# Performance work log

Hardware: AMD Instinct MI355X
Metric: run time of the kernel (lower is better)

## Reference

```python
import jax, jax.numpy as jnp
import numpy as np

D_INP=36; D_MODEL=144; NHEAD=4; NHID=128; NLAYERS=2
MAX_LEN=215; D_STATIC=9; D_PE=16; N_CLASSES=2; B=128
D_OB=D_MODEL//D_INP; GCH=MAX_LEN*D_OB; D_TR=D_MODEL+D_PE; D_FINAL=D_TR+D_INP
_EI=np.stack(np.nonzero(np.ones((D_INP,D_INP),dtype=np.int64)))  # torch.nonzero(ones).T -> all pairs
SRC_N=jnp.asarray(_EI[0]); TGT_N=jnp.asarray(_EI[1]); N_EDGE=_EI.shape[1]


def setup_inputs():
    ks=jax.random.split(jax.random.key(0),40)
    def w(i,shape,s=0.05): return jax.random.normal(ks[i],shape,jnp.float32)*s
    return {
      'src': jax.random.normal(ks[0],(MAX_LEN,B,2*D_INP),jnp.float32),
      'static': jax.random.normal(ks[1],(B,D_STATIC),jnp.float32),
      'times': jax.random.uniform(ks[2],(MAX_LEN,B),jnp.float32)*MAX_LEN,
      'lengths': jax.random.randint(ks[3],(B,),32,MAX_LEN+1),
      'R_u': w(4,(1,D_INP*D_OB)),
      'emb_w': w(5,(D_INP,D_STATIC)), 'emb_b': jnp.zeros(D_INP,jnp.float32),
      'Wv1': w(6,(GCH,GCH),1.0/np.sqrt(GCH)), 'bv1': jnp.zeros(GCH,jnp.float32),
      'Wv2': w(7,(GCH,GCH),1.0/np.sqrt(GCH)), 'bv2': jnp.zeros(GCH,jnp.float32),
      'in_proj_w': w(8,(NLAYERS,3*D_TR,D_TR)), 'in_proj_b': jnp.zeros((NLAYERS,3*D_TR),jnp.float32),
      'out_w': w(9,(NLAYERS,D_TR,D_TR)), 'out_b': jnp.zeros((NLAYERS,D_TR),jnp.float32),
      'lin1_w': w(10,(NLAYERS,NHID,D_TR)), 'lin1_b': jnp.zeros((NLAYERS,NHID),jnp.float32),
      'lin2_w': w(11,(NLAYERS,D_TR,NHID)), 'lin2_b': jnp.zeros((NLAYERS,D_TR),jnp.float32),
      'ln1_s': jnp.ones((NLAYERS,D_TR),jnp.float32), 'ln1_b': jnp.zeros((NLAYERS,D_TR),jnp.float32),
      'ln2_s': jnp.ones((NLAYERS,D_TR),jnp.float32), 'ln2_b': jnp.zeros((NLAYERS,D_TR),jnp.float32),
      'mlp1_w': w(12,(D_FINAL,D_FINAL)), 'mlp1_b': jnp.zeros(D_FINAL,jnp.float32),
      'mlp2_w': w(13,(N_CLASSES,D_FINAL)), 'mlp2_b': jnp.zeros(N_CLASSES,jnp.float32),
    }


def _seg_softmax(wgt, seg, n):
    m=jnp.full((n,),-jnp.inf,wgt.dtype).at[seg].max(wgt)
    e=jnp.exp(wgt-m[seg])
    s=jnp.zeros((n,),wgt.dtype).at[seg].add(e)
    return e/s[seg]


def _ln(x,s,b):
    mu=jnp.mean(x,-1,keepdims=True); v=jnp.var(x,-1,keepdims=True)
    return (x-mu)/jnp.sqrt(v+1e-5)*s+b


def _forward(src, static, times, R_u, emb_w, emb_b, Wv1, bv1, Wv2, bv2, in_proj_w, in_proj_b, out_w, out_b, lin1_w, lin1_b, lin2_w, lin2_b, ln1_s, ln1_b, ln2_s, ln2_b, mlp1_w, mlp1_b, mlp2_w, mlp2_b, lengths):
    T,Bb=src.shape[0],src.shape[1]
    obs=src[:,:,:D_INP]                                  # drop mask half
    h=jax.nn.relu(jnp.repeat(obs,D_OB,axis=-1)*R_u)      # h_u = relu(x_u*R_u), [T,B,144]
    ts=jnp.asarray(MAX_LEN**np.linspace(0,1,D_PE//2),jnp.float32)
    scaled=times[:,:,None]/ts
    pe=jnp.concatenate([jnp.sin(scaled),jnp.cos(scaled)],-1)  # [T,B,16]
    emb=static@emb_w.T+emb_b                             # [B,36]
    # --- Observation_progation x2 (use_beta=False): gather-softmax-scatter per sensor graph ---
    xb=h.transpose(1,0,2).reshape(Bb,T,D_INP,D_OB).transpose(0,2,1,3).reshape(Bb,D_INP,GCH)
    ew=jnp.ones((N_EDGE,),jnp.float32)                   # adj=ones -> edge_weights=1
    gamma=_seg_softmax(ew,TGT_N,D_INP)                   # softmax over edges per target node
    def prop(x_,Wv,bv):
        V=jax.nn.relu(x_@Wv.T+bv)                        # relu(lin_value(x_j))
        msgs=V[:,SRC_N,:]*gamma[None,:,None]             # gather source features per edge
        return jnp.zeros_like(x_).at[:,TGT_N,:].add(msgs)  # scatter-add to targets
    x1=prop(xb,Wv1,bv1)
    x2=prop(x1,Wv2,bv2)                                  # layer2 uses alpha1 = raw edge_weights
    alpha=jnp.broadcast_to(ew[None,:],(Bb,N_EDGE))       # alpha_all.T
    sq=jnp.sum(alpha*alpha,1)
    d2=jnp.maximum(sq[:,None]+sq[None,:]-2.0*(alpha@alpha.T),0.0)
    distance=jnp.mean(jnp.sqrt(d2))
    out=x2.reshape(Bb,D_INP,T,D_OB).transpose(2,0,1,3).reshape(T,Bb,D_INP*D_OB)
    x=jnp.concatenate([out,pe],-1)                       # [T,B,160]
    mask=jnp.arange(T)[None,:]>=lengths[:,None]          # [B,T] True = padded
    hd=D_TR//NHEAD
    for l in range(NLAYERS):                             # torch post-norm TransformerEncoderLayer
        qkv=x@in_proj_w[l].T+in_proj_b[l]
        q,k,v=jnp.split(qkv,3,-1)
        def heads(t): return t.reshape(T,Bb,NHEAD,hd).transpose(1,2,0,3)  # [B,H,T,hd]
        sc=jnp.einsum('bhqd,bhkd->bhqk',heads(q),heads(k))/np.sqrt(hd)
        sc=jnp.where(mask[:,None,None,:],jnp.float32(-1e30),sc)
        o=jnp.einsum('bhqk,bhkd->bhqd',jax.nn.softmax(sc,-1),heads(v))
        o=o.transpose(2,0,1,3).reshape(T,Bb,D_TR)@out_w[l].T+out_b[l]
        x=_ln(x+o,ln1_s[l],ln1_b[l])
        ff=jax.nn.relu(x@lin1_w[l].T+lin1_b[l])@lin2_w[l].T+lin2_b[l]
        x=_ln(x+ff,ln2_s[l],ln2_b[l])
    valid=1.0-mask.T[:,:,None].astype(x.dtype)           # [T,B,1]
    agg=jnp.sum(x*valid,0)/(lengths[:,None].astype(x.dtype)+1.0)
    feat=jnp.concatenate([agg,emb],1)                    # [B,196]
    logits=jax.nn.relu(feat@mlp1_w.T+mlp1_b)@mlp2_w.T+mlp2_b
    return logits,distance


def reference(src, static, times, lengths, R_u, emb_w, emb_b, Wv1, bv1, Wv2, bv2, in_proj_w, in_proj_b, out_w, out_b, lin1_w, lin1_b, lin2_w, lin2_b, ln1_s, ln1_b, ln2_s, ln2_b, mlp1_w, mlp1_b, mlp2_w, mlp2_b):
    return _forward(src, static, times, R_u, emb_w, emb_b, Wv1, bv1, Wv2, bv2, in_proj_w, in_proj_b, out_w, out_b, lin1_w, lin1_b, lin2_w, lin2_b, ln1_s, ln1_b, ln2_s, ln2_b, mlp1_w, mlp1_b, mlp2_w, mlp2_b, lengths)
```

## Files before the change

kernel.cpp:

```cpp
#include <hip/hip_runtime.h>
#include <math.h>

#define T_LEN 215
#define TP    224
#define B_N   128
#define DINP  36
#define D_TR  160
#define HD    40
#define D_FIN 196
#define KPG   864

typedef __attribute__((ext_vector_type(8))) short short8v;
typedef __attribute__((ext_vector_type(4))) float f32x4;

__device__ __forceinline__ ushort f2bf(float x) {
  union { float f; unsigned u; } c; c.f = x;
  unsigned r = c.u + 0x7fffu + ((c.u >> 16) & 1u);
  return (ushort)(r >> 16);
}
__device__ __forceinline__ float bf2f(ushort h) {
  union { unsigned u; float f; } c; c.u = ((unsigned)h) << 16;
  return c.f;
}

__global__ __launch_bounds__(256) void k_prep(const float* __restrict__ Wv1,
    const float* __restrict__ Wv2, const float* __restrict__ ipw, const float* __restrict__ ow,
    const float* __restrict__ l1w, const float* __restrict__ l2w,
    const float* __restrict__ src, const float* __restrict__ R_u,
    const float* __restrict__ stat, const float* __restrict__ emb_w, const float* __restrict__ emb_b,
    ushort* __restrict__ wv1b, ushort* __restrict__ wv2b, ushort* __restrict__ ipwb,
    ushort* __restrict__ owb, ushort* __restrict__ l1wb, ushort* __restrict__ l2wb,
    float* __restrict__ v2acc, float* __restrict__ featacc,
    ushort* __restrict__ obuf16, ushort* __restrict__ xb16) {
  __shared__ float Ss[T_LEN * DINP];
  if (blockIdx.x >= 8202) {
    const int b = blockIdx.x - 8202, tid = threadIdx.x;
    for (int i = tid; i < T_LEN * DINP; i += 256) {
      int t = i / DINP, j = i - t * DINP;
      Ss[i] = src[((size_t)t * B_N + b) * 72 + j];
    }
    __syncthreads();
    for (int i = tid; i < DINP * T_LEN; i += 256) {
      int ii = i / T_LEN, t = i - ii * T_LEN;
      float v = Ss[t * DINP + ii];
      float4 r = ((const float4*)R_u)[ii];
      ushort4 o;
      o.x = f2bf(fmaxf(v * r.x, 0.f)); o.y = f2bf(fmaxf(v * r.y, 0.f));
      o.z = f2bf(fmaxf(v * r.z, 0.f)); o.w = f2bf(fmaxf(v * r.w, 0.f));
      ushort* row = xb16 + (size_t)(b * DINP + ii) * KPG;
      *(ushort4*)(row + 4 * t) = o;
      if (t == 0) { ushort4 z = {0, 0, 0, 0}; *(ushort4*)(row + 860) = z; }
    }
    return;
  }
  int i = blockIdx.x * 256 + threadIdx.x;
  if (i < 746496) { int n = i / KPG, k = i % KPG;
    wv1b[i] = (n < 860 && k < 860) ? f2bf(Wv1[n * 860 + k]) : (ushort)0; return; }
  i -= 746496;
  if (i < 746496) { int n = i / KPG, k = i % KPG;
    wv2b[i] = (n < 860 && k < 860) ? f2bf(Wv2[n * 860 + k]) : (ushort)0; return; }
  i -= 746496;
  if (i < 153600) { ipwb[i] = f2bf(ipw[i]); return; }
  i -= 153600;
  if (i < 51200)  { owb[i] = f2bf(ow[i]); return; }
  i -= 51200;
  if (i < 40960)  { l1wb[i] = f2bf(l1w[i]); return; }
  i -= 40960;
  if (i < 40960)  { l2wb[i] = f2bf(l2w[i]); return; }
  i -= 40960;
  if (i < 110592) { v2acc[i] = 0.f; return; }
  i -= 110592;
  if (i < 20480)  { int b = i / D_TR, d = i - b * D_TR;
    featacc[b * D_FIN + d] = 0.f; return; }
  i -= 20480;
  if (i < 4608)   { int b = i / DINP, ii = i - b * DINP;
    float s = emb_b[ii];
    #pragma unroll
    for (int k = 0; k < 9; k++) s = fmaf(stat[b * 9 + k], emb_w[ii * 9 + k], s);
    featacc[b * D_FIN + D_TR + ii] = s; return; }
  i -= 4608;
  if (i < 184320) {
    int b = i / 1440, rem = i % 1440;
    int t = 215 + rem / 160, cc = rem % 160;
    obuf16[((size_t)b * TP + t) * D_TR + cc] = 0; return;
  }
}

__global__ __launch_bounds__(256) void k_red_s1(const ushort* __restrict__ V1b, ushort* __restrict__ s1) {
  int idx = blockIdx.x * 256 + threadIdx.x;
  if (idx >= B_N * KPG) return;
  int b = idx / KPG, n = idx % KPG;
  float s = 0.f;
  if (n < 860) {
    #pragma unroll 4
    for (int i = 0; i < DINP; i++) s += bf2f(V1b[((size_t)b * DINP + i) * 860 + n]);
    s *= (1.0f / 36.0f);
  }
  s1[idx] = (n < 860) ? f2bf(s) : (ushort)0;
}

__global__ __launch_bounds__(256) void k_buildx(const float* __restrict__ v2acc,
    const float* __restrict__ bv2, const float* __restrict__ times,
    ushort* __restrict__ x16) {
  int idx = blockIdx.x * 256 + threadIdx.x;
  if (idx >= B_N * TP * 40) return;
  int c = idx % 40;
  int r = idx / 40;
  int t = r % TP, b = r / TP;
  float4 f = {0.f, 0.f, 0.f, 0.f};
  if (t < T_LEN) {
    if (c < 36) {
      float4 a = *(const float4*)&v2acc[(size_t)b * KPG + 4 * t];
      float4 bb = *(const float4*)&bv2[4 * t];
      f.x = fmaxf(a.x + bb.x, 0.f); f.y = fmaxf(a.y + bb.y, 0.f);
      f.z = fmaxf(a.z + bb.z, 0.f); f.w = fmaxf(a.w + bb.w, 0.f);
    } else {
      float tm = times[t * B_N + b];
      int j0 = (c - 36) * 4;
      bool is_sin = j0 < 8;
      int kb = j0 & 7;
      float o[4];
      #pragma unroll
      for (int qq = 0; qq < 4; qq++) {
        float ts = expf((float)(kb + qq) * 0.76723400f);
        float sc = tm / ts;
        o[qq] = is_sin ? sinf(sc) : cosf(sc);
      }
      f.x = o[0]; f.y = o[1]; f.z = o[2]; f.w = o[3];
    }
  }
  ushort4 h = {f2bf(f.x), f2bf(f.y), f2bf(f.z), f2bf(f.w)};
  *(ushort4*)(x16 + (size_t)r * D_TR + 4 * c) = h;
}

template <int RELU, int SPLIT, int WMODE, int BNT>
__global__ __launch_bounds__(256) void gemm_bf16(const ushort* __restrict__ A,
    const ushort* __restrict__ W, const float* __restrict__ bias, void* __restrict__ Cv,
    int KP, int ldc, int ncols, int kts) {
  __shared__ ushort As[128 * 32];
  __shared__ ushort Ws[BNT * 32];
  constexpr int NJ = BNT / 16;
  const int tid = threadIdx.x;
  const int wave = tid >> 6, lane = tid & 63;
  const int lr = lane & 15, hi = lane >> 4;
  const int m0 = blockIdx.y * 128, n0 = blockIdx.x * BNT;
  const int kt0 = blockIdx.z * kts;

  f32x4 acc[2][NJ];
  #pragma unroll
  for (int i = 0; i < 2; i++)
    #pragma unroll
    for (int j = 0; j < NJ; j++) acc[i][j] = (f32x4){0.f, 0.f, 0.f, 0.f};

  const int ar = tid >> 2, g = tid & 3;
  const size_t abase0 = (size_t)(m0 + ar) * KP;
  const size_t abase1 = (size_t)(m0 + ar + 64) * KP;
  const size_t bbase0 = (size_t)(n0 + ar) * KP;
  const size_t bbase1 = (size_t)(n0 + ar + 64) * KP;
  const int awb0 = ar * 64 + ((g * 16) ^ ((ar & 3) << 4));
  const int awb1 = awb0 + 64 * 64;

  const int arow0 = wave * 32 + lr;
  const int arb0 = arow0 * 64 + ((hi * 16) ^ ((arow0 & 3) << 4));
  const int arb1 = (arow0 + 16) * 64 + ((hi * 16) ^ (((arow0 + 16) & 3) << 4));
  int brb[NJ];
  #pragma unroll
  for (int j = 0; j < NJ; j++)
    brb[j] = (j * 16 + lr) * 64 + ((hi * 16) ^ ((lr & 3) << 4));

  for (int kt = 0; kt < kts; ++kt) {
    const int k0 = (kt0 + kt) * 32;
    uint4 va0 = *(const uint4*)(A + abase0 + k0 + g * 8);
    uint4 va1 = *(const uint4*)(A + abase1 + k0 + g * 8);
    uint4 vb0 = *(const uint4*)(W + bbase0 + k0 + g * 8);
    uint4 vb1;
    if constexpr (BNT == 128) vb1 = *(const uint4*)(W + bbase1 + k0 + g * 8);
    if (kt) __syncthreads();
    *(uint4*)((char*)As + awb0) = va0;
    *(uint4*)((char*)As + awb1) = va1;
    *(uint4*)((char*)Ws + awb0) = vb0;
    if constexpr (BNT == 128) *(uint4*)((char*)Ws + awb1) = vb1;
    __syncthreads();
    short8v a0 = *(const short8v*)((const char*)As + arb0);
    short8v a1 = *(const short8v*)((const char*)As + arb1);
    #pragma unroll
    for (int j = 0; j < NJ; j++) {
      short8v bf = *(const short8v*)((const char*)Ws + brb[j]);
      acc[0][j] = __builtin_amdgcn_mfma_f32_16x16x32_bf16(a0, bf, acc[0][j], 0, 0, 0);
      acc[1][j] = __builtin_amdgcn_mfma_f32_16x16x32_bf16(a1, bf, acc[1][j], 0, 0, 0);
    }
  }

  #pragma unroll
  for (int i = 0; i < 2; i++) {
    #pragma unroll
    for (int j = 0; j < NJ; j++) {
      int col = n0 + j * 16 + lr;
      int row = m0 + wave * 32 + i * 16 + hi * 4;
      if (col < ncols) {
        if constexpr (SPLIT) {
          #pragma unroll
          for (int r = 0; r < 4; r++)
            atomicAdd((float*)Cv + (size_t)(row + r) * ldc + col, acc[i][j][r]);
        } else {
          float bb = bias ? bias[col] : 0.f;
          #pragma unroll
          for (int r = 0; r < 4; r++) {
            float xv = acc[i][j][r] + bb;
            if (RELU) xv = fmaxf(xv, 0.f);
            if (WMODE == 0) ((float*)Cv)[(size_t)(row + r) * ldc + col] = xv;
            else            ((ushort*)Cv)[(size_t)(row + r) * ldc + col] = f2bf(xv);
          }
        }
      }
    }
  }
}

__global__ __launch_bounds__(256) void gemm_qkv(const ushort* __restrict__ A,
    const ushort* __restrict__ W, const float* __restrict__ bias,
    ushort* __restrict__ qkvB, ushort* __restrict__ Vt, int kts) {
  __shared__ ushort As[128 * 32];
  __shared__ ushort Ws[128 * 32];
  const int KP = 160;
  const int tid = threadIdx.x;
  const int wave = tid >> 6, lane = tid & 63;
  const int lr = lane & 15, hi = lane >> 4;
  const int m0 = blockIdx.y * 128, n0 = blockIdx.x * 128;

  f32x4 acc[2][8];
  #pragma unroll
  for (int i = 0; i < 2; i++)
    #pragma unroll
    for (int j = 0; j < 8; j++) acc[i][j] = (f32x4){0.f, 0.f, 0.f, 0.f};

  const int ar = tid >> 2, g = tid & 3;
  const size_t abase0 = (size_t)(m0 + ar) * KP;
  const size_t abase1 = (size_t)(m0 + ar + 64) * KP;
  const size_t bbase0 = (size_t)(n0 + ar) * KP;
  const size_t bbase1 = (size_t)(n0 + ar + 64) * KP;
  const int awb0 = ar * 64 + ((g * 16) ^ ((ar & 3) << 4));
  const int awb1 = awb0 + 64 * 64;

  const int arow0 = wave * 32 + lr;
  const int arb0 = arow0 * 64 + ((hi * 16) ^ ((arow0 & 3) << 4));
  const int arb1 = (arow0 + 16) * 64 + ((hi * 16) ^ (((arow0 + 16) & 3) << 4));
  int brb[8];
  #pragma unroll
  for (int j = 0; j < 8; j++)
    brb[j] = (j * 16 + lr) * 64 + ((hi * 16) ^ ((lr & 3) << 4));

  for (int kt = 0; kt < kts; ++kt) {
    const int k0 = kt * 32;
    uint4 va0 = *(const uint4*)(A + abase0 + k0 + g * 8);
    uint4 va1 = *(const uint4*)(A + abase1 + k0 + g * 8);
    uint4 vb0 = *(const uint4*)(W + bbase0 + k0 + g * 8);
    uint4 vb1 = *(const uint4*)(W + bbase1 + k0 + g * 8);
    if (kt) __syncthreads();
    *(uint4*)((char*)As + awb0) = va0;
    *(uint4*)((char*)As + awb1) = va1;
    *(uint4*)((char*)Ws + awb0) = vb0;
    *(uint4*)((char*)Ws + awb1) = vb1;
    __syncthreads();
    short8v a0 = *(const short8v*)((const char*)As + arb0);
    short8v a1 = *(const short8v*)((const char*)As + arb1);
    #pragma unroll
    for (int j = 0; j < 8; j++) {
      short8v bf = *(const short8v*)((const char*)Ws + brb[j]);
      acc[0][j] = __builtin_amdgcn_mfma_f32_16x16x32_bf16(a0, bf, acc[0][j], 0, 0, 0);
      acc[1][j] = __builtin_amdgcn_mfma_f32_16x16x32_bf16(a1, bf, acc[1][j], 0, 0, 0);
    }
  }

  #pragma unroll
  for (int i = 0; i < 2; i++) {
    const int row = m0 + wave * 32 + i * 16 + hi * 4;
    const int b = row / TP, t0 = row - b * TP;
    #pragma unroll
    for (int j = 0; j < 8; j++) {
      int col = n0 + j * 16 + lr;
      if (col < 320) {
        float bb = bias[col];
        #pragma unroll
        for (int r = 0; r < 4; r++)
          qkvB[(size_t)(row + r) * 480 + col] = f2bf(acc[i][j][r] + bb);
      } else if (col < 480) {
        float bb = bias[col];
        int dg = col - 320;
        int hh = dg / 40, dd = dg - hh * 40;
        ushort4 pv;
        pv.x = f2bf(acc[i][j][0] + bb); pv.y = f2bf(acc[i][j][1] + bb);
        pv.z = f2bf(acc[i][j][2] + bb); pv.w = f2bf(acc[i][j][3] + bb);
        *(ushort4*)(Vt + (((size_t)(b * 4 + hh) * 48 + dd) * TP + t0)) = pv;
      }
    }
  }
}

__global__ __launch_bounds__(256) void gemm_lnff(const ushort* __restrict__ Ao,
    const ushort* __restrict__ Wo, const float* __restrict__ bo,
    const float* __restrict__ g1, const float* __restrict__ be1,
    const ushort* __restrict__ W1, const float* __restrict__ b1,
    const ushort* __restrict__ W2, const float* __restrict__ b2,
    const float* __restrict__ g2, const float* __restrict__ be2,
    ushort* __restrict__ x16, const int* __restrict__ lengths,
    float* __restrict__ featacc) {
  __shared__ ushort As[64 * 32];
  __shared__ ushort Ws[160 * 32];
  __shared__ ushort W1s[128 * 32];
  __shared__ ushort W2s[160 * 32];
  __shared__ ushort Xln[64 * 168];
  __shared__ ushort Hs[64 * 136];
  const int tid = threadIdx.x;
  const int wave = tid >> 6, lane = tid & 63;
  const int lr = lane & 15, hi = lane >> 4;
  const int m0 = blockIdx.x * 64;

  const int ar = tid >> 2, g = tid & 3;
  const int awb = ar * 64 + ((g * 16) ^ ((ar & 3) << 4));
  const int awb1 = awb + 64 * 64;
  const int wr0 = tid >> 2,         ws0 = tid & 3;
  const int wr1 = (tid + 256) >> 2, ws1 = (tid + 256) & 3;
  const int wr2 = (tid + 512) >> 2, ws2 = (tid + 512) & 3;
  const int wwb0 = wr0 * 64 + ((ws0 * 16) ^ ((wr0 & 3) << 4));
  const int wwb1 = wr1 * 64 + ((ws1 * 16) ^ ((wr1 & 3) << 4));
  const int wwb2 = wr2 * 64 + ((ws2 * 16) ^ ((wr2 & 3) << 4));
  const int arow = wave * 16 + lr;
  const int arb = arow * 64 + ((hi * 16) ^ ((arow & 3) << 4));
  int brb[10];
  #pragma unroll
  for (int j = 0; j < 10; j++)
    brb[j] = (j * 16 + lr) * 64 + ((hi * 16) ^ ((lr & 3) << 4));

  const int lrow0 = wave * 16 + hi * 4;
  const int rb = m0 + lrow0;

  {
    f32x4 acc[10];
    #pragma unroll
    for (int j = 0; j < 10; j++) acc[j] = (f32x4){0.f, 0.f, 0.f, 0.f};
    const size_t abase = (size_t)(m0 + ar) * 160;
    for (int kt = 0; kt < 5; ++kt) {
      const int k0 = kt * 32;
      uint4 va = *(const uint4*)(Ao + abase + k0 + g * 8);
      uint4 w0 = *(const uint4*)(Wo + (size_t)wr0 * 160 + k0 + ws0 * 8);
      uint4 w1 = *(const uint4*)(Wo + (size_t)wr1 * 160 + k0 + ws1 * 8);
      uint4 w2;
      if (tid < 128) w2 = *(const uint4*)(Wo + (size_t)wr2 * 160 + k0 + ws2 * 8);
      if (kt) __syncthreads();
      *(uint4*)((char*)As + awb) = va;
      *(uint4*)((char*)Ws + wwb0) = w0;
      *(uint4*)((char*)Ws + wwb1) = w1;
      if (tid < 128) *(uint4*)((char*)Ws + wwb2) = w2;
      __syncthreads();
      short8v a0 = *(const short8v*)((const char*)As + arb);
      #pragma unroll
      for (int j = 0; j < 10; j++) {
        short8v bf = *(const short8v*)((const char*)Ws + brb[j]);
        acc[j] = __builtin_amdgcn_mfma_f32_16x16x32_bf16(a0, bf, acc[j], 0, 0, 0);
      }
    }
    float s[4] = {0.f, 0.f, 0.f, 0.f};
    #pragma unroll
    for (int j = 0; j < 10; j++) {
      const int col = j * 16 + lr;
      const float bb = bo[col];
      #pragma unroll
      for (int r = 0; r < 4; r++) {
        float v = acc[j][r] + bb + bf2f(x16[(size_t)(rb + r) * D_TR + col]);
        acc[j][r] = v;
        s[r] += v;
      }
    }
    #pragma unroll
    for (int r = 0; r < 4; r++) {
      s[r] += __shfl_xor(s[r], 1, 64);
      s[r] += __shfl_xor(s[r], 2, 64);
      s[r] += __shfl_xor(s[r], 4, 64);
      s[r] += __shfl_xor(s[r], 8, 64);
    }
    float mu[4], q2[4] = {0.f, 0.f, 0.f, 0.f};
    #pragma unroll
    for (int r = 0; r < 4; r++) mu[r] = s[r] * (1.0f / 160.0f);
    #pragma unroll
    for (int j = 0; j < 10; j++)
      #pragma unroll
      for (int r = 0; r < 4; r++) {
        float d = acc[j][r] - mu[r];
        q2[r] += d * d;
      }
    #pragma unroll
    for (int r = 0; r < 4; r++) {
      q2[r] += __shfl_xor(q2[r], 1, 64);
      q2[r] += __shfl_xor(q2[r], 2, 64);
      q2[r] += __shfl_xor(q2[r], 4, 64);
      q2[r] += __shfl_xor(q2[r], 8, 64);
    }
    float rstd[4];
    #pragma unroll
    for (int r = 0; r < 4; r++) rstd[r] = rsqrtf(q2[r] * (1.0f / 160.0f) + 1e-5f);
    #pragma unroll
    for (int j = 0; j < 10; j++) {
      const int col = j * 16 + lr;
      const float gc = g1[col], bc = be1[col];
      #pragma unroll
      for (int r = 0; r < 4; r++) {
        float o = (acc[j][r] - mu[r]) * rstd[r] * gc + bc;
        Xln[(lrow0 + r) * 168 + col] = f2bf(o);
      }
    }
  }
  __syncthreads();

  {
    f32x4 acc1[8];
    #pragma unroll
    for (int j = 0; j < 8; j++) acc1[j] = (f32x4){0.f, 0.f, 0.f, 0.f};
    int brb8[8];
    #pragma unroll
    for (int j = 0; j < 8; j++)
      brb8[j] = (j * 16 + lr) * 64 + ((hi * 16) ^ ((lr & 3) << 4));
    for (int kt = 0; kt < 5; ++kt) {
      const int k0 = kt * 32;
      uint4 w10 = *(const uint4*)(W1 + (size_t)ar * 160 + k0 + g * 8);
      uint4 w11 = *(const uint4*)(W1 + (size_t)(ar + 64) * 160 + k0 + g * 8);
      if (kt) __syncthreads();
      *(uint4*)((char*)W1s + awb) = w10;
      *(uint4*)((char*)W1s + awb1) = w11;
      __syncthreads();
      short8v a0 = *(const short8v*)(&Xln[(wave * 16 + lr) * 168 + k0 + hi * 8]);
      #pragma unroll
      for (int j = 0; j < 8; j++) {
        short8v bf = *(const short8v*)((const char*)W1s + brb8[j]);
        acc1[j] = __builtin_amdgcn_mfma_f32_16x16x32_bf16(a0, bf, acc1[j], 0, 0, 0);
      }
    }
    #pragma unroll
    for (int j = 0; j < 8; j++) {
      const int col = j * 16 + lr;
      const float bb = b1[col];
      #pragma unroll
      for (int r = 0; r < 4; r++)
        Hs[(lrow0 + r) * 136 + col] = f2bf(fmaxf(acc1[j][r] + bb, 0.f));
    }
  }
  __syncthreads();

  {
    f32x4 acc[10];
    #pragma unroll
    for (int j = 0; j < 10; j++) acc[j] = (f32x4){0.f, 0.f, 0.f, 0.f};
    for (int kt = 0; kt < 4; ++kt) {
      const int k0 = kt * 32;
      uint4 w0 = *(const uint4*)(W2 + (size_t)wr0 * 128 + k0 + ws0 * 8);
      uint4 w1 = *(const uint4*)(W2 + (size_t)wr1 * 128 + k0 + ws1 * 8);
      uint4 w2;
      if (tid < 128) w2 = *(const uint4*)(W2 + (size_t)wr2 * 128 + k0 + ws2 * 8);
      if (kt) __syncthreads();
      *(uint4*)((char*)W2s + wwb0) = w0;
      *(uint4*)((char*)W2s + wwb1) = w1;
      if (tid < 128) *(uint4*)((char*)W2s + wwb2) = w2;
      __syncthreads();
      short8v a0 = *(const short8v*)(&Hs[(wave * 16 + lr) * 136 + k0 + hi * 8]);
      #pragma unroll
      for (int j = 0; j < 10; j++) {
        short8v bf = *(const short8v*)((const char*)W2s + brb[j]);
        acc[j] = __builtin_amdgcn_mfma_f32_16x16x32_bf16(a0, bf, acc[j], 0, 0, 0);
      }
    }
    float s[4] = {0.f, 0.f, 0.f, 0.f};
    #pragma unroll
    for (int j = 0; j < 10; j++) {
      const int col = j * 16 + lr;
      const float bb = b2[col];
      #pragma unroll
      for (int r = 0; r < 4; r++) {
        float v = acc[j][r] + bb + bf2f(Xln[(lrow0 + r) * 168 + col]);
        acc[j][r] = v;
        s[r] += v;
      }
    }
    #pragma unroll
    for (int r = 0; r < 4; r++) {
      s[r] += __shfl_xor(s[r], 1, 64);
      s[r] += __shfl_xor(s[r], 2, 64);
      s[r] += __shfl_xor(s[r], 4, 64);
      s[r] += __shfl_xor(s[r], 8, 64);
    }
    float mu[4], q2[4] = {0.f, 0.f, 0.f, 0.f};
    #pragma unroll
    for (int r = 0; r < 4; r++) mu[r] = s[r] * (1.0f / 160.0f);
    #pragma unroll
    for (int j = 0; j < 10; j++)
      #pragma unroll
      for (int r = 0; r < 4; r++) {
        float d = acc[j][r] - mu[r];
        q2[r] += d * d;
      }
    #pragma unroll
    for (int r = 0; r < 4; r++) {
      q2[r] += __shfl_xor(q2[r], 1, 64);
      q2[r] += __shfl_xor(q2[r], 2, 64);
      q2[r] += __shfl_xor(q2[r], 4, 64);
      q2[r] += __shfl_xor(q2[r], 8, 64);
    }
    float rstd[4];
    #pragma unroll
    for (int r = 0; r < 4; r++) rstd[r] = rsqrtf(q2[r] * (1.0f / 160.0f) + 1e-5f);

    if (featacc == nullptr) {
      #pragma unroll
      for (int j = 0; j < 10; j++) {
        const int col = j * 16 + lr;
        const float gc = g2[col], bc = be2[col];
        #pragma unroll
        for (int r = 0; r < 4; r++) {
          float o = (acc[j][r] - mu[r]) * rstd[r] * gc + bc;
          x16[(size_t)(rb + r) * D_TR + col] = f2bf(o);
        }
      }
    } else {
      const int b = rb / TP, t0 = rb - b * TP;
      int L = lengths[b]; if (L > T_LEN) L = T_LEN;
      #pragma unroll
      for (int j = 0; j < 10; j++) {
        const int col = j * 16 + lr;
        const float gc = g2[col], bc = be2[col];
        float sacc = 0.f;
        #pragma unroll
        for (int r = 0; r < 4; r++) {
          float o = (acc[j][r] - mu[r]) * rstd[r] * gc + bc;
          if (t0 + r < L) sacc += o;
        }
        if (t0 < L) atomicAdd(&featacc[b * D_FIN + col], sacc);
      }
    }
  }
}

__global__ __launch_bounds__(64) void k_attn4(const ushort* __restrict__ qkvB,
    const ushort* __restrict__ Vt, const int* __restrict__ lengths,
    ushort* __restrict__ o16) {
  __shared__ ushort SP[16 * 232];
  const int bh = blockIdx.x;
  const int b = bh >> 2, h = bh & 3;
  int L = lengths[b]; if (L > T_LEN) L = T_LEN;
  const int q0 = blockIdx.y << 4;
  if (q0 >= L) return;
  const int lane = threadIdx.x;
  const int lr = lane & 15, hi = lane >> 4;
  const int nk16 = (L + 15) >> 4;
  const int nkt  = (L + 31) >> 5;
  const float SC = 0.15811388300841898f;

  const ushort* qrow = qkvB + ((size_t)b * TP + q0) * 480 + h * 40;
  uint4 qa0u = *(const uint4*)(qrow + lr * 480 + hi * 8);
  uint4 qa1u = {0, 0, 0, 0};
  if (hi == 0) qa1u = *(const uint4*)(qrow + lr * 480 + 32);
  short8v qa0 = *(short8v*)&qa0u;
  short8v qa1 = *(short8v*)&qa1u;

  f32x4 c[14];
  #pragma unroll
  for (int kt = 0; kt < 14; ++kt) {
    c[kt] = (f32x4){0.f, 0.f, 0.f, 0.f};
    if (kt < nk16) {
      const ushort* krow = qkvB + ((size_t)b * TP + kt * 16) * 480 + 160 + h * 40;
      uint4 kb0u = *(const uint4*)(krow + lr * 480 + hi * 8);
      uint4 kb1u = {0, 0, 0, 0};
      if (hi == 0) kb1u = *(const uint4*)(krow + lr * 480 + 32);
      c[kt] = __builtin_amdgcn_mfma_f32_16x16x32_bf16(qa0, *(short8v*)&kb0u, c[kt], 0, 0, 0);
      c[kt] = __builtin_amdgcn_mfma_f32_16x16x32_bf16(qa1, *(short8v*)&kb1u, c[kt], 0, 0, 0);
    }
  }

  float mx[4] = {-1e30f, -1e30f, -1e30f, -1e30f};
  #pragma unroll
  for (int kt = 0; kt < 14; ++kt) {
    if (kt < nk16) {
      bool valid = (kt * 16 + lr) < L;
      #pragma unroll
      for (int r = 0; r < 4; r++) {
        float v = valid ? c[kt][r] : -1e30f;
        mx[r] = fmaxf(mx[r], v);
      }
    }
  }
  #pragma unroll
  for (int r = 0; r < 4; r++) {
    mx[r] = fmaxf(mx[r], __shfl_xor(mx[r], 1, 64));
    mx[r] = fmaxf(mx[r], __shfl_xor(mx[r], 2, 64));
    mx[r] = fmaxf(mx[r], __shfl_xor(mx[r], 4, 64));
    mx[r] = fmaxf(mx[r], __shfl_xor(mx[r], 8, 64));
  }
  float sum[4] = {0.f, 0.f, 0.f, 0.f};
  #pragma unroll
  for (int kt = 0; kt < 14; ++kt) {
    if (kt < nk16) {
      bool valid = (kt * 16 + lr) < L;
      #pragma unroll
      for (int r = 0; r < 4; r++) {
        float p = valid ? __expf(SC * (c[kt][r] - mx[r])) : 0.f;
        sum[r] += p;
        c[kt][r] = p;
      }
    }
  }
  #pragma unroll
  for (int r = 0; r < 4; r++) {
    sum[r] += __shfl_xor(sum[r], 1, 64);
    sum[r] += __shfl_xor(sum[r], 2, 64);
    sum[r] += __shfl_xor(sum[r], 4, 64);
    sum[r] += __shfl_xor(sum[r], 8, 64);
  }

  const int nk16w = nkt * 2;
  #pragma unroll
  for (int kt = 0; kt < 14; ++kt) {
    if (kt < nk16w) {
      #pragma unroll
      for (int r = 0; r < 4; r++)
        SP[(hi * 4 + r) * 232 + kt * 16 + lr] = f2bf(c[kt][r]);
    }
  }
  __syncthreads();

  f32x4 o0 = {0.f, 0.f, 0.f, 0.f}, o1 = o0, o2 = o0;
  const ushort* vbase = Vt + (size_t)bh * 48 * TP;
  #pragma unroll
  for (int kt = 0; kt < 7; ++kt) {
    if (kt < nkt) {
      short8v pa = *(const short8v*)((const char*)SP + lr * 464 + kt * 64 + hi * 16);
      const ushort* vb = vbase + kt * 32 + hi * 8;
      short8v v0 = *(const short8v*)(vb + (size_t)lr * TP);
      short8v v1 = *(const short8v*)(vb + (size_t)(16 + lr) * TP);
      short8v v2 = *(const short8v*)(vb + (size_t)(32 + lr) * TP);
      o0 = __builtin_amdgcn_mfma_f32_16x16x32_bf16(pa, v0, o0, 0, 0, 0);
      o1 = __builtin_amdgcn_mfma_f32_16x16x32_bf16(pa, v1, o1, 0, 0, 0);
      o2 = __builtin_amdgcn_mfma_f32_16x16x32_bf16(pa, v2, o2, 0, 0, 0);
    }
  }

  #pragma unroll
  for (int r = 0; r < 4; r++) {
    int t = q0 + hi * 4 + r;
    if (t < T_LEN) {
      float inv = 1.0f / sum[r];
      ushort* op = o16 + ((size_t)b * TP + t) * D_TR + h * 40;
      op[lr]      = f2bf(o0[r] * inv);
      op[16 + lr] = f2bf(o1[r] * inv);
      if (lr < 8) op[32 + lr] = f2bf(o2[r] * inv);
    }
  }
}

__global__ __launch_bounds__(256) void k_head2(const float* __restrict__ featacc,
    const int* __restrict__ lengths, const float* __restrict__ m1w,
    const float* __restrict__ m1b, const float* __restrict__ m2w,
    const float* __restrict__ m2b, float* __restrict__ out) {
  __shared__ float feat[196];
  __shared__ float m1o_s[196];
  __shared__ float r0[4], r1[4];
  const int b = blockIdx.x, tid = threadIdx.x;
  int L = lengths[b]; if (L > T_LEN) L = T_LEN;
  const float inv = 1.0f / (float)(L + 1);
  if (tid < D_FIN)
    feat[tid] = featacc[(size_t)b * D_FIN + tid] * (tid < D_TR ? inv : 1.f);
  __syncthreads();
  if (tid < D_FIN) {
    float s = m1b[tid];
    const float* wr = m1w + (size_t)tid * D_FIN;
    #pragma unroll 4
    for (int k = 0; k < D_FIN; k++) s = fmaf(feat[k], wr[k], s);
    m1o_s[tid] = fmaxf(s, 0.f);
  }
  __syncthreads();
  float p0 = 0.f, p1 = 0.f;
  if (tid < D_FIN) {
    p0 = m1o_s[tid] * m2w[tid];
    p1 = m1o_s[tid] * m2w[D_FIN + tid];
  }
  #pragma unroll
  for (int off = 32; off; off >>= 1) {
    p0 += __shfl_xor(p0, off, 64);
    p1 += __shfl_xor(p1, off, 64);
  }
  int w = tid >> 6;
  if ((tid & 63) == 0) { r0[w] = p0; r1[w] = p1; }
  __syncthreads();
  if (tid == 0) out[2 * b]     = r0[0] + r0[1] + r0[2] + r0[3] + m2b[0];
  if (tid == 1) out[2 * b + 1] = r1[0] + r1[1] + r1[2] + r1[3] + m2b[1];
  if (b == 0 && tid == 2) out[256] = 0.f;
}

extern "C" void kernel_launch(void* const* d_in, const int* in_sizes, int n_in,
                              void* d_out, int out_size, void* d_ws, size_t ws_size,
                              hipStream_t stream) {
  const float* src   = (const float*)d_in[0];
  const float* stat  = (const float*)d_in[1];
  const float* times = (const float*)d_in[2];
  const int*   lens  = (const int*)d_in[3];
  const float* R_u   = (const float*)d_in[4];
  const float* emb_w = (const float*)d_in[5];
  const float* emb_b = (const float*)d_in[6];
  const float* Wv1   = (const float*)d_in[7];
  const float* bv1   = (const float*)d_in[8];
  const float* Wv2   = (const float*)d_in[9];
  const float* bv2   = (const float*)d_in[10];
  const float* ipw   = (const float*)d_in[11];
  const float* ipb   = (const float*)d_in[12];
  const float* ow    = (const float*)d_in[13];
  const float* ob    = (const float*)d_in[14];
  const float* l1w   = (const float*)d_in[15];
  const float* l1b   = (const float*)d_in[16];
  const float* l2w   = (const float*)d_in[17];
  const float* l2b   = (const float*)d_in[18];
  const float* ln1s  = (const float*)d_in[19];
  const float* ln1bb = (const float*)d_in[20];
  const float* ln2s  = (const float*)d_in[21];
  const float* ln2bb = (const float*)d_in[22];
  const float* m1w   = (const float*)d_in[23];
  const float* m1b   = (const float*)d_in[24];
  const float* m2w   = (const float*)d_in[25];
  const float* m2b   = (const float*)d_in[26];
  float* out = (float*)d_out;

  char* p = (char*)d_ws;
  ushort* x16    = (ushort*)p;  p += 9175040;
  float*  v2acc  = (float*)p;   p += 442368;
  ushort* s1b    = (ushort*)p;  p += 221184;
  ushort* obuf16 = (ushort*)p;  p += 9175040;
  ushort* wv1b   = (ushort*)p;  p += 1492992;
  ushort* wv2b   = (ushort*)p;  p += 1492992;
  ushort* ipwb   = (ushort*)p;  p += 307200;
  ushort* owb    = (ushort*)p;  p += 102400;
  ushort* l1wb   = (ushort*)p;  p += 81920;
  ushort* l2wb   = (ushort*)p;  p += 81920;
  float*  featacc= (float*)p;   p += 100352;
  char*   R2     = p;
  ushort* xb16   = (ushort*)R2;
  ushort* V1b    = (ushort*)(R2 + 7962624);
  ushort* qkvB   = (ushort*)R2;
  ushort* Vt     = (ushort*)(R2 + 27525120);

  k_prep<<<8330, 256, 0, stream>>>(Wv1, Wv2, ipw, ow, l1w, l2w, src, R_u,
                                   stat, emb_w, emb_b,
                                   wv1b, wv2b, ipwb, owb, l1wb, l2wb,
                                   v2acc, featacc, obuf16, xb16);

  gemm_bf16<1, 0, 1, 128><<<dim3(7, 36, 1), 256, 0, stream>>>(
      xb16, wv1b, bv1, V1b, KPG, 860, 860, 27);
  k_red_s1<<<432, 256, 0, stream>>>(V1b, s1b);
  gemm_bf16<0, 1, 0, 64><<<dim3(14, 1, 9), 256, 0, stream>>>(
      s1b, wv2b, nullptr, v2acc, KPG, KPG, KPG, 3);
  k_buildx<<<4480, 256, 0, stream>>>(v2acc, bv2, times, x16);

  for (int l = 0; l < 2; l++) {
    gemm_qkv<<<dim3(4, 224, 1), 256, 0, stream>>>(
        x16, ipwb + (size_t)l * 76800, ipb + l * 480, qkvB, Vt, 5);
    k_attn4<<<dim3(512, 14), 64, 0, stream>>>(qkvB, Vt, lens, obuf16);
    gemm_lnff<<<448, 256, 0, stream>>>(
        obuf16, owb + (size_t)l * 25600, ob + l * 160,
        ln1s + l * 160, ln1bb + l * 160,
        l1wb + (size_t)l * 20480, l1b + l * 128,
        l2wb + (size_t)l * 20480, l2b + l * 160,
        ln2s + l * 160, ln2bb + l * 160,
        x16, lens, (l == 1) ? featacc : nullptr);
  }

  k_head2<<<128, 256, 0, stream>>>(featacc, lens, m1w, m1b, m2w, m2b, out);
}
```

Measured before the change: 225.4 us.

## Fuse graph reduction, second GEMV and input build into one per-batch kernel

Replaces the separate reduction, split-K atomic GEMM and input-build kernels with a single per-batch kernel that reduces V1 in shared memory, computes the second projection as a wave-level GEMV, and writes the transformer input directly. This removes two launches, the v2acc zeroing and the atomics, and the global round trips of the intermediates. The first GEMM also switches to 64-wide N tiles to get more blocks. The cost is that the fused kernel runs only 128 blocks and each one streams the full Wv2 matrix, so it relies on cache reuse and has limited parallelism.

New measurement: 682.5 us. 3.03x slower.

```diff
diff --git a/kernel.cpp b/kernel.cpp
--- a/kernel.cpp
+++ b/kernel.cpp
@@ -30,11 +30,10 @@
     const float* __restrict__ stat, const float* __restrict__ emb_w, const float* __restrict__ emb_b,
     ushort* __restrict__ wv1b, ushort* __restrict__ wv2b, ushort* __restrict__ ipwb,
     ushort* __restrict__ owb, ushort* __restrict__ l1wb, ushort* __restrict__ l2wb,
-    float* __restrict__ v2acc, float* __restrict__ featacc,
-    ushort* __restrict__ obuf16, ushort* __restrict__ xb16) {
+    float* __restrict__ featacc, ushort* __restrict__ obuf16, ushort* __restrict__ xb16) {
   __shared__ float Ss[T_LEN * DINP];
-  if (blockIdx.x >= 8202) {
-    const int b = blockIdx.x - 8202, tid = threadIdx.x;
+  if (blockIdx.x >= 7770) {
+    const int b = blockIdx.x - 7770, tid = threadIdx.x;
     for (int i = tid; i < T_LEN * DINP; i += 256) {
       int t = i / DINP, j = i - t * DINP;
       Ss[i] = src[((size_t)t * B_N + b) * 72 + j];
@@ -68,8 +67,6 @@
   i -= 40960;
   if (i < 40960)  { l2wb[i] = f2bf(l2w[i]); return; }
   i -= 40960;
-  if (i < 110592) { v2acc[i] = 0.f; return; }
-  i -= 110592;
   if (i < 20480)  { int b = i / D_TR, d = i - b * D_TR;
     featacc[b * D_FIN + d] = 0.f; return; }
   i -= 20480;
@@ -86,54 +83,78 @@
   }
 }
 
-__global__ __launch_bounds__(256) void k_red_s1(const ushort* __restrict__ V1b, ushort* __restrict__ s1) {
-  int idx = blockIdx.x * 256 + threadIdx.x;
-  if (idx >= B_N * KPG) return;
-  int b = idx / KPG, n = idx % KPG;
-  float s = 0.f;
-  if (n < 860) {
-    #pragma unroll 4
-    for (int i = 0; i < DINP; i++) s += bf2f(V1b[((size_t)b * DINP + i) * 860 + n]);
-    s *= (1.0f / 36.0f);
-  }
-  s1[idx] = (n < 860) ? f2bf(s) : (ushort)0;
-}
-
-__global__ __launch_bounds__(256) void k_buildx(const float* __restrict__ v2acc,
-    const float* __restrict__ bv2, const float* __restrict__ times,
-    ushort* __restrict__ x16) {
-  int idx = blockIdx.x * 256 + threadIdx.x;
-  if (idx >= B_N * TP * 40) return;
-  int c = idx % 40;
-  int r = idx / 40;
-  int t = r % TP, b = r / TP;
-  float4 f = {0.f, 0.f, 0.f, 0.f};
-  if (t < T_LEN) {
-    if (c < 36) {
-      float4 a = *(const float4*)&v2acc[(size_t)b * KPG + 4 * t];
-      float4 bb = *(const float4*)&bv2[4 * t];
-      f.x = fmaxf(a.x + bb.x, 0.f); f.y = fmaxf(a.y + bb.y, 0.f);
-      f.z = fmaxf(a.z + bb.z, 0.f); f.w = fmaxf(a.w + bb.w, 0.f);
-    } else {
-      float tm = times[t * B_N + b];
-      int j0 = (c - 36) * 4;
-      bool is_sin = j0 < 8;
-      int kb = j0 & 7;
-      float o[4];
-      #pragma unroll
-      for (int qq = 0; qq < 4; qq++) {
-        float ts = expf((float)(kb + qq) * 0.76723400f);
-        float sc = tm / ts;
-        o[qq] = is_sin ? sinf(sc) : cosf(sc);
-      }
-      f.x = o[0]; f.y = o[1]; f.z = o[2]; f.w = o[3];
-    }
-  }
-  ushort4 h = {f2bf(f.x), f2bf(f.y), f2bf(f.z), f2bf(f.w)};
-  *(ushort4*)(x16 + (size_t)r * D_TR + 4 * c) = h;
-}
-
-template <int RELU, int SPLIT, int WMODE, int BNT>
+__global__ __launch_bounds__(256) void k_graphtail(const ushort* __restrict__ V1b,
+    const ushort* __restrict__ wv2b, const float* __restrict__ bv2,
+    const float* __restrict__ times, ushort* __restrict__ x16) {
+  __shared__ ushort s1l[KPG];
+  __shared__ float  v2l[KPG];
+  const int b = blockIdx.x, tid = threadIdx.x;
+  const int wave = tid >> 6, lane = tid & 63;
+
+  for (int n = tid; n < KPG; n += 256) {
+    float s = 0.f;
+    if (n < 860) {
+      #pragma unroll 4
+      for (int i = 0; i < DINP; i++) s += bf2f(V1b[((size_t)(b * DINP + i)) * 860 + n]);
+      s *= (1.0f / 36.0f);
+    }
+    s1l[n] = f2bf(s);
+  }
+  __syncthreads();
+
+  {
+    const int nbase = wave * 216;
+    for (int nn = 0; nn < 216; nn += 2) {
+      const int n0 = nbase + nn, n1 = n0 + 1;
+      const ushort* w0 = wv2b + (size_t)n0 * KPG;
+      const ushort* w1 = wv2b + (size_t)n1 * KPG;
+      float a0 = 0.f, a1 = 0.f;
+      for (int k = lane; k < KPG; k += 64) {
+        float sv = bf2f(s1l[k]);
+        a0 = fmaf(sv, bf2f(w0[k]), a0);
+        a1 = fmaf(sv, bf2f(w1[k]), a1);
+      }
+      #pragma unroll
+      for (int off = 32; off; off >>= 1) {
+        a0 += __shfl_xor(a0, off, 64);
+        a1 += __shfl_xor(a1, off, 64);
+      }
+      if (lane == 0) { v2l[n0] = a0; v2l[n1] = a1; }
+    }
+  }
+  __syncthreads();
+
+  for (int idx = tid; idx < TP * 40; idx += 256) {
+    int c = idx % 40, t = idx / 40;
+    float4 f = {0.f, 0.f, 0.f, 0.f};
+    if (t < T_LEN) {
+      if (c < 36) {
+        float4 bb = *(const float4*)&bv2[4 * t];
+        f.x = fmaxf(v2l[4 * t]     + bb.x, 0.f);
+        f.y = fmaxf(v2l[4 * t + 1] + bb.y, 0.f);
+        f.z = fmaxf(v2l[4 * t + 2] + bb.z, 0.f);
+        f.w = fmaxf(v2l[4 * t + 3] + bb.w, 0.f);
+      } else {
+        float tm = times[t * B_N + b];
+        int j0 = (c - 36) * 4;
+        bool is_sin = j0 < 8;
+        int kb = j0 & 7;
+        float o[4];
+        #pragma unroll
+        for (int qq = 0; qq < 4; qq++) {
+          float ts = expf((float)(kb + qq) * 0.76723400f);
+          float sc = tm / ts;
+          o[qq] = is_sin ? sinf(sc) : cosf(sc);
+        }
+        f.x = o[0]; f.y = o[1]; f.z = o[2]; f.w = o[3];
+      }
+    }
+    ushort4 h = {f2bf(f.x), f2bf(f.y), f2bf(f.z), f2bf(f.w)};
+    *(ushort4*)(x16 + ((size_t)b * TP + t) * D_TR + 4 * c) = h;
+  }
+}
+
+template <int RELU, int WMODE, int BNT>
 __global__ __launch_bounds__(256) void gemm_bf16(const ushort* __restrict__ A,
     const ushort* __restrict__ W, const float* __restrict__ bias, void* __restrict__ Cv,
     int KP, int ldc, int ncols, int kts) {
@@ -144,7 +165,6 @@
   const int wave = tid >> 6, lane = tid & 63;
   const int lr = lane & 15, hi = lane >> 4;
   const int m0 = blockIdx.y * 128, n0 = blockIdx.x * BNT;
-  const int kt0 = blockIdx.z * kts;
 
   f32x4 acc[2][NJ];
   #pragma unroll
@@ -169,7 +189,7 @@
     brb[j] = (j * 16 + lr) * 64 + ((hi * 16) ^ ((lr & 3) << 4));
 
   for (int kt = 0; kt < kts; ++kt) {
-    const int k0 = (kt0 + kt) * 32;
+    const int k0 = kt * 32;
     uint4 va0 = *(const uint4*)(A + abase0 + k0 + g * 8);
     uint4 va1 = *(const uint4*)(A + abase1 + k0 + g * 8);
     uint4 vb0 = *(const uint4*)(W + bbase0 + k0 + g * 8);
@@ -198,19 +218,13 @@
       int col = n0 + j * 16 + lr;
       int row = m0 + wave * 32 + i * 16 + hi * 4;
       if (col < ncols) {
-        if constexpr (SPLIT) {
-          #pragma unroll
-          for (int r = 0; r < 4; r++)
-            atomicAdd((float*)Cv + (size_t)(row + r) * ldc + col, acc[i][j][r]);
-        } else {
-          float bb = bias ? bias[col] : 0.f;
-          #pragma unroll
-          for (int r = 0; r < 4; r++) {
-            float xv = acc[i][j][r] + bb;
-            if (RELU) xv = fmaxf(xv, 0.f);
-            if (WMODE == 0) ((float*)Cv)[(size_t)(row + r) * ldc + col] = xv;
-            else            ((ushort*)Cv)[(size_t)(row + r) * ldc + col] = f2bf(xv);
-          }
+        float bb = bias ? bias[col] : 0.f;
+        #pragma unroll
+        for (int r = 0; r < 4; r++) {
+          float xv = acc[i][j][r] + bb;
+          if (RELU) xv = fmaxf(xv, 0.f);
+          if (WMODE == 0) ((float*)Cv)[(size_t)(row + r) * ldc + col] = xv;
+          else            ((ushort*)Cv)[(size_t)(row + r) * ldc + col] = f2bf(xv);
         }
       }
     }
@@ -727,8 +741,6 @@
 
   char* p = (char*)d_ws;
   ushort* x16    = (ushort*)p;  p += 9175040;
-  float*  v2acc  = (float*)p;   p += 442368;
-  ushort* s1b    = (ushort*)p;  p += 221184;
   ushort* obuf16 = (ushort*)p;  p += 9175040;
   ushort* wv1b   = (ushort*)p;  p += 1492992;
   ushort* wv2b   = (ushort*)p;  p += 1492992;
@@ -743,17 +755,14 @@
   ushort* qkvB   = (ushort*)R2;
   ushort* Vt     = (ushort*)(R2 + 27525120);
 
-  k_prep<<<8330, 256, 0, stream>>>(Wv1, Wv2, ipw, ow, l1w, l2w, src, R_u,
+  k_prep<<<7898, 256, 0, stream>>>(Wv1, Wv2, ipw, ow, l1w, l2w, src, R_u,
                                    stat, emb_w, emb_b,
                                    wv1b, wv2b, ipwb, owb, l1wb, l2wb,
-                                   v2acc, featacc, obuf16, xb16);
-
-  gemm_bf16<1, 0, 1, 128><<<dim3(7, 36, 1), 256, 0, stream>>>(
+                                   featacc, obuf16, xb16);
+
+  gemm_bf16<1, 1, 64><<<dim3(14, 36, 1), 256, 0, stream>>>(
       xb16, wv1b, bv1, V1b, KPG, 860, 860, 27);
-  k_red_s1<<<432, 256, 0, stream>>>(V1b, s1b);
-  gemm_bf16<0, 1, 0, 64><<<dim3(14, 1, 9), 256, 0, stream>>>(
-      s1b, wv2b, nullptr, v2acc, KPG, KPG, KPG, 3);
-  k_buildx<<<4480, 256, 0, stream>>>(v2acc, bv2, times, x16);
+  k_graphtail<<<128, 256, 0, stream>>>(V1b, wv2b, bv2, times, x16);
 
   for (int l = 0; l < 2; l++) {
     gemm_qkv<<<dim3(4, 224, 1), 256, 0, stream>>>(
```
